# Optimization experiments

Measured on AMD Instinct MI355X. Metric: run time of the kernel, lower is better.

The kernel has to match this reference:

```python
import jax, jax.numpy as jnp
import numpy as np

TEMPERATURE = 0.8
TOP_K = 50
TOP_P = 0.9
REP_PENALTY = 1.2
FILTER_VALUE = -1e9  # stands in for -inf in HF top_k_top_p_filtering (numerically identical probs)

B, S, V = 16, 64, 50257
P = 64  # previously generated tokens per sequence


def setup_inputs() -> dict:
    key = jax.random.key(0)
    k1, k2 = jax.random.split(key)
    logits = jax.random.normal(k1, (B, S, V), dtype=jnp.float32) * 3.0
    prev_tokens = jax.random.randint(k2, (S, P), 0, V)
    return {"logits": logits, "prev_tokens": prev_tokens}


def _repetition_penalty(logits, prev_tokens):
    # logits: [B,S,V], prev_tokens: [S,P]
    gathered = jnp.take_along_axis(logits, prev_tokens[None, :, :], axis=-1)  # [B,S,P]
    all_neg = jnp.all(gathered < 0, axis=0, keepdims=True)                    # [1,S,P]
    penalized = jnp.where(all_neg, gathered * REP_PENALTY, gathered / REP_PENALTY)
    s_idx = jnp.broadcast_to(jnp.arange(S)[:, None], prev_tokens.shape)       # [S,P]
    # scatter back (duplicate indices write identical values -> matches set() semantics)
    return logits.at[:, s_idx, prev_tokens].set(penalized)


def _top_k_top_p_filter(logits):
    # top-k: mask everything below the k-th largest logit
    if TOP_K > 0:
        kth = jax.lax.top_k(logits, TOP_K)[0][..., -1:]                       # [B,S,1]
        logits = jnp.where(logits < kth, FILTER_VALUE, logits)
    # top-p (nucleus): sort descending, mask tokens past cumulative prob TOP_P
    if TOP_P < 1.0:
        sort_idx = jnp.argsort(-logits, axis=-1)                              # [B,S,V]
        sorted_logits = jnp.take_along_axis(logits, sort_idx, axis=-1)
        cum_probs = jnp.cumsum(jax.nn.softmax(sorted_logits, axis=-1), axis=-1)
        remove_sorted = cum_probs > TOP_P
        # shift right so the first token exceeding the threshold is kept
        remove_sorted = jnp.concatenate(
            [jnp.zeros_like(remove_sorted[..., :1]), remove_sorted[..., :-1]], axis=-1)
        inv_idx = jnp.argsort(sort_idx, axis=-1)
        remove = jnp.take_along_axis(remove_sorted, inv_idx, axis=-1)
        logits = jnp.where(remove, FILTER_VALUE, logits)
    return logits


def reference(logits, prev_tokens):
    if REP_PENALTY != 1.0:
        logits = _repetition_penalty(logits, prev_tokens)
    logits = logits / TEMPERATURE
    logits = _top_k_top_p_filter(logits)
    # Categorical(logits=...) normalizes logits; return normalized log-probs
    return jax.nn.log_softmax(logits, axis=-1)
```

## Files before the change

### kernel.cpp

```cpp
#include <hip/hip_runtime.h>
#include <cstdint>
#include <cfloat>
#include <math.h>

#define BB 16
#define SS 64
#define VV 50257
#define PP 64

#define NT 512
#define BINS 2048
#define CAP 1536
#define BMW 1572
#define KCAP 128
#define BCAP 512
#define TRAW 6.0f

typedef float f32x4 __attribute__((ext_vector_type(4)));

__device__ __forceinline__ uint32_t fkey(float f) {
    uint32_t u = __float_as_uint(f);
    return u ^ ((uint32_t)((int32_t)u >> 31) | 0x80000000u);
}
__device__ __forceinline__ float key2f(uint32_t u) {
    uint32_t b = (u & 0x80000000u) ? (u ^ 0x80000000u) : ~u;
    return __uint_as_float(b);
}

__global__ __launch_bounds__(NT)
void sch_kernel(const float* __restrict__ logits,
                const int* __restrict__ prev,
                float* __restrict__ out)
{
    const int r   = blockIdx.x;
    const int b   = r / SS;
    const int s   = r % SS;
    const int tid = threadIdx.x;
    const float* row  = logits + (size_t)r * VV;
    float*       orow = out    + (size_t)r * VV;

    __shared__ uint32_t s_bm[BMW];
    __shared__ float    s_cv[CAP];
    __shared__ int      s_ci[CAP];
    __shared__ uint32_t s_hist[BINS];
    __shared__ uint32_t s_scan[16];
    __shared__ int      s_ptok[PP];
    __shared__ float    s_ppen[PP];
    __shared__ float    s_praw[PP];
    __shared__ int      s_pneg[PP];
    __shared__ float    s_binv[BCAP];
    __shared__ double   s_v64[KCAP];
    __shared__ double   s_e64[KCAP];
    __shared__ int      s_ki[KCAP];
    __shared__ float    s_kof[KCAP];
    __shared__ int    s_cnt, s_cntinv, s_b50, s_need, s_cntb, s_k50, s_kp, s_Kk;
    __shared__ float  s_kth, s_rc;
    __shared__ double s_lse;

    for (int i = tid; i < BMW; i += NT) s_bm[i] = 0u;
    if (tid < PP) s_pneg[tid] = 1;
    if (tid == 0) { s_cnt = 0; s_cntinv = 0; }
    __syncthreads();
    for (int pair = tid; pair < PP * BB; pair += NT) {
        int ti = pair & (PP - 1);
        int b2 = pair >> 6;
        int tok = prev[s * PP + ti];
        float g = logits[((size_t)b2 * SS + s) * (size_t)VV + tok];
        if (g >= 0.f) atomicAnd(&s_pneg[ti], 0);
        if (b2 == b) { s_praw[ti] = g; s_ptok[ti] = tok; }
    }
    __syncthreads();
    if (tid < PP) {
        float gown = s_praw[tid];
        float pen = s_pneg[tid] ? (gown * 1.2f) : (gown / 1.2f);
        s_ppen[tid] = pen;
        int tok = s_ptok[tid];
        atomicOr(&s_bm[tok >> 5], 1u << (tok & 31));
    }
    __syncthreads();

    const int mis   = (int)(((size_t)row >> 2) & 3);
    const int head  = (4 - mis) & 3;
    const int nq    = (VV - head) >> 2;
    const int ttail = head + (nq << 2);
    const float4* p4 = reinterpret_cast<const float4*>(row + head);

    auto kbit = [&](int t) -> uint32_t {
        return (s_bm[t >> 5] >> (t & 31)) & 1u;
    };
    auto addRaw = [&](int t, float raw) {
        if (raw >= TRAW) {
            int pos = atomicAdd(&s_cnt, 1);
            if (pos < CAP) { s_cv[pos] = raw; s_ci[pos] = t; }
        }
    };
    auto streamFast = [&]() {
        for (int t = tid; t < head; t += NT) addRaw(t, row[t]);
        int base = 0;
        for (; base + 4 * NT <= nq; base += 4 * NT) {
            float4 f[4];
            #pragma unroll
            for (int u = 0; u < 4; ++u) f[u] = p4[base + tid + u * NT];
            #pragma unroll
            for (int u = 0; u < 4; ++u) {
                int t = head + ((base + tid + u * NT) << 2);
                addRaw(t + 0, f[u].x);
                addRaw(t + 1, f[u].y);
                addRaw(t + 2, f[u].z);
                addRaw(t + 3, f[u].w);
            }
        }
        for (int q = base + tid; q < nq; q += NT) {
            float4 f = p4[q];
            int t = head + (q << 2);
            addRaw(t + 0, f.x);
            addRaw(t + 1, f.y);
            addRaw(t + 2, f.z);
            addRaw(t + 3, f.w);
        }
        for (int t = ttail + tid; t < VV; t += NT) addRaw(t, row[t]);
    };
    auto procFull = [&](int t, float raw, bool doHist, float thr) {
        float v = raw;
        if (kbit(t)) {
            #pragma unroll 1
            for (int j = 0; j < PP; ++j)
                if (s_ptok[j] == t) { v = s_ppen[j]; break; }
        }
        if (!doHist) {
            if (v >= thr) {
                int pos = atomicAdd(&s_cnt, 1);
                if (pos < CAP) { s_cv[pos] = v; s_ci[pos] = t; }
            }
        } else {
            atomicAdd(&s_hist[fkey(v) >> 21], 1u);
        }
    };
    auto streamFull = [&](bool doHist, float thr) {
        for (int t = tid; t < head; t += NT) procFull(t, row[t], doHist, thr);
        for (int q = tid; q < nq; q += NT) {
            float4 f = p4[q];
            int t = head + (q << 2);
            procFull(t + 0, f.x, doHist, thr);
            procFull(t + 1, f.y, doHist, thr);
            procFull(t + 2, f.z, doHist, thr);
            procFull(t + 3, f.w, doHist, thr);
        }
        for (int t = ttail + tid; t < VV; t += NT) procFull(t, row[t], doHist, thr);
    };
    auto findB50 = [&](int target) {
        __syncthreads();
        const int per = BINS / NT;
        int base = tid * per;
        uint32_t loc = 0;
        #pragma unroll
        for (int k2 = 0; k2 < per; ++k2) loc += s_hist[base + k2];
        uint32_t incl = loc;
        #pragma unroll
        for (int off = 1; off < 64; off <<= 1) {
            uint32_t u = (uint32_t)__shfl_up((int)incl, off, 64);
            if ((tid & 63) >= off) incl += u;
        }
        int wid = tid >> 6;
        if ((tid & 63) == 63) s_scan[wid] = incl;
        __syncthreads();
        if (tid < 8) {
            uint32_t p = 0;
            for (int w = 0; w < tid; ++w) p += s_scan[w];
            s_scan[8 + tid] = p;
        }
        __syncthreads();
        uint32_t pre_incl = s_scan[8 + wid] + incl;
        uint32_t total    = s_scan[8 + 7] + s_scan[7];
        uint32_t run = total - pre_incl;
        for (int k2 = per - 1; k2 >= 0; --k2) {
            uint32_t h = s_hist[base + k2];
            uint32_t run2 = run + h;
            if (run < (uint32_t)target && run2 >= (uint32_t)target) {
                s_b50 = base + k2;
                s_need = target - (int)run;
            }
            run = run2;
        }
        __syncthreads();
    };
    auto doFallback = [&]() {
        for (int i = tid; i < BINS; i += NT) s_hist[i] = 0u;
        __syncthreads();
        streamFull(true, 0.f);
        findB50(50);
        float thrF = key2f((uint32_t)s_b50 << 21);
        if (tid == 0) s_cnt = 0;
        __syncthreads();
        streamFull(false, thrF);
        __syncthreads();
    };
    auto computeKth = [&]() {
        for (int i = tid; i < BINS; i += NT) s_hist[i] = 0u;
        if (tid == 0) { s_cntb = 0; s_kth = -FLT_MAX; }
        __syncthreads();
        int cc = min(s_cnt, CAP);
        for (int i = tid; i < cc; i += NT)
            atomicAdd(&s_hist[fkey(s_cv[i]) >> 21], 1u);
        findB50(50);
        int b50 = s_b50, need = s_need;
        for (int i = tid; i < cc; i += NT) {
            if ((int)(fkey(s_cv[i]) >> 21) == b50) {
                int p = atomicAdd(&s_cntb, 1);
                if (p < BCAP) s_binv[p] = s_cv[i];
            }
        }
        __syncthreads();
        int cb = min(s_cntb, BCAP);
        for (int i = tid; i < cb; i += NT) {
            float vi = s_binv[i];
            int gt = 0, ge = 0;
            for (int j = 0; j < cb; ++j) {
                float vj = s_binv[j];
                gt += (vj > vi);
                ge += (vj >= vi);
            }
            if (gt < need && ge >= need) s_kth = vi;
        }
        __syncthreads();
    };

    streamFast();
    __syncthreads();
    const int cntRaw = min(s_cnt, CAP);
    for (int i = tid; i < cntRaw; i += NT) {
        if (kbit(s_ci[i])) {
            s_cv[i] = -FLT_MAX;
            atomicAdd(&s_cntinv, 1);
        }
    }
    __syncthreads();
    if (tid < PP) {
        int tok = s_ptok[tid];
        bool first = true;
        for (int j = 0; j < tid; ++j)
            if (s_ptok[j] == tok) { first = false; break; }
        if (first) {
            int pos = atomicAdd(&s_cnt, 1);
            if (pos < CAP) { s_cv[pos] = s_ppen[tid]; s_ci[pos] = tok; }
        }
    }
    __syncthreads();
    bool fellback = false;
    {
        bool okc = (s_cnt <= CAP) && ((cntRaw - s_cntinv) >= 50);
        if (!okc) { doFallback(); fellback = true; }
    }

    computeKth();
    if (!fellback && (s_kth - 1e-4f < TRAW)) {
        doFallback();
        computeKth();
    }
    if (tid == 0) s_k50 = 0;
    __syncthreads();
    const float kth = s_kth;

    const float gthr = kth - 1e-4f;
    const int cntc = min(s_cnt, CAP);
    for (int i = tid; i < cntc; i += NT) {
        if (s_cv[i] >= gthr) {
            int p = atomicAdd(&s_k50, 1);
            if (p < KCAP) {
                int tok = s_ci[i];
                double v64;
                if (kbit(tok)) {
                    int pj = 0;
                    #pragma unroll 1
                    for (int j = 0; j < PP; ++j)
                        if (s_ptok[j] == tok) { pj = j; break; }
                    double g = (double)s_praw[pj];
                    double pen = s_pneg[pj] ? (g * 1.2) : (g / 1.2);
                    v64 = pen / 0.8;
                } else {
                    v64 = (double)s_cv[i] / 0.8;
                }
                s_v64[p] = v64;
                s_ki[p]  = tok;
            }
        }
    }
    __syncthreads();
    const int k50c = min(s_k50, KCAP);
    for (int i = k50c + tid; i < KCAP; i += NT) {
        s_v64[i] = -1e300;
        s_ki[i]  = (1 << 30) + i;
    }
    __syncthreads();

    if (tid < 64) {
        int l = tid;
        double v0 = s_v64[l],    v1 = s_v64[l + 64];
        int    i0 = s_ki[l],     i1 = s_ki[l + 64];
        for (int k = 2; k <= KCAP; k <<= 1) {
            for (int j = k >> 1; j > 0; j >>= 1) {
                if (j >= 64) {
                    bool before = (v0 > v1) || (v0 == v1 && i0 < i1);
                    if (!before) {
                        double tv = v0; v0 = v1; v1 = tv;
                        int    ti = i0; i0 = i1; i1 = ti;
                    }
                } else {
                    double nv0 = __shfl_xor(v0, j, 64);
                    double nv1 = __shfl_xor(v1, j, 64);
                    int    ni0 = __shfl_xor(i0, j, 64);
                    int    ni1 = __shfl_xor(i1, j, 64);
                    bool lower = ((l & j) == 0);
                    bool up0 = ((l & k) == 0);
                    bool up1 = (((l + 64) & k) == 0);
                    bool bm0 = (v0 > nv0) || (v0 == nv0 && i0 < ni0);
                    bool bm1 = (v1 > nv1) || (v1 == nv1 && i1 < ni1);
                    bool keep0 = lower ? (up0 == bm0) : (up0 != bm0);
                    bool keep1 = lower ? (up1 == bm1) : (up1 != bm1);
                    if (!keep0) { v0 = nv0; i0 = ni0; }
                    if (!keep1) { v1 = nv1; i1 = ni1; }
                }
            }
        }
        s_v64[l] = v0; s_v64[l + 64] = v1;
        s_ki[l]  = i0; s_ki[l + 64]  = i1;
    }
    __syncthreads();

    if (tid == 0) {
        int kk = k50c;
        int Kkept;
        if (kk <= 50) Kkept = kk;
        else {
            double kth64 = s_v64[49];
            Kkept = 50;
            while (Kkept < kk && s_v64[Kkept] == kth64) ++Kkept;
        }
        s_Kk = Kkept;
    }
    __syncthreads();
    const int Kk = s_Kk;
    const double mx = s_v64[0];
    if (tid < Kk) s_e64[tid] = exp(s_v64[tid] - mx);
    __syncthreads();
    if (tid == 0) {
        double D = 0.0;
        #pragma unroll 1
        for (int i = 0; i < Kk; ++i) D += s_e64[i];
        double c = 0.0;
        int Kp = 0;
        #pragma unroll 1
        for (int i = 0; i < Kk; ++i) {
            bool keep = (i == 0) || (c <= 0.9);
            c += s_e64[i] / D;
            if (keep) Kp = i + 1; else break;
        }
        double D2 = 0.0;
        #pragma unroll 1
        for (int i = 0; i < Kp; ++i) D2 += s_e64[i];
        double lse = log(D2);
        s_lse = lse;
        s_rc = (float)((-1e9 - mx) - lse);
        s_kp = Kp;
    }
    __syncthreads();
    if (tid < s_kp) s_kof[tid] = (float)((s_v64[tid] - mx) - s_lse);

    const float rc = s_rc;
    {
        const int omis   = (int)(((size_t)orow >> 2) & 3);
        const int ohead  = (4 - omis) & 3;
        const int onq    = (VV - ohead) >> 2;
        const int ottail = ohead + (onq << 2);
        f32x4* o4 = reinterpret_cast<f32x4*>(orow + ohead);
        f32x4 rc4; rc4.x = rc; rc4.y = rc; rc4.z = rc; rc4.w = rc;
        for (int t = tid; t < ohead; t += NT)
            __builtin_nontemporal_store(rc, &orow[t]);
        for (int q = tid; q < onq; q += NT)
            __builtin_nontemporal_store(rc4, &o4[q]);
        for (int t = ottail + tid; t < VV; t += NT)
            __builtin_nontemporal_store(rc, &orow[t]);
    }
    __syncthreads();
    if (tid < s_kp) orow[s_ki[tid]] = s_kof[tid];
}

extern "C" void kernel_launch(void* const* d_in, const int* in_sizes, int n_in,
                              void* d_out, int out_size, void* d_ws, size_t ws_size,
                              hipStream_t stream) {
    const float* logits = (const float*)d_in[0];
    const int*   prev   = (const int*)d_in[1];
    float*       out    = (float*)d_out;
    dim3 grid(BB * SS), block(NT);
    hipLaunchKernelGGL(sch_kernel, grid, block, 0, stream, logits, prev, out);
}
```

Measured before the change: 99.40 us.

## Process two rows per block, overlapping row A output stores with row B loads

Each block now handles two rows, rA and rA+512, which share the same sequence index, and the grid shrinks from 1024 to 512 blocks. The repetition-penalty gather for those rows is done once and yields penalties for both. The fill store of row A's output is interleaved with the streaming read and candidate collection of row B, so reads and writes overlap inside one block. In exchange, each block does its work serially across two rows with fewer blocks in flight, which may cut latency hiding and parallelism across the CUs.

```diff
diff --git a/kernel.cpp b/kernel.cpp
--- a/kernel.cpp
+++ b/kernel.cpp
@@ -9,6 +9,7 @@
 #define PP 64
 
 #define NT 512
+#define NBLK 512
 #define BINS 2048
 #define CAP 1536
 #define BMW 1572
@@ -32,12 +33,17 @@
                 const int* __restrict__ prev,
                 float* __restrict__ out)
 {
-    const int r   = blockIdx.x;
-    const int b   = r / SS;
-    const int s   = r % SS;
+    const int g   = blockIdx.x;
+    const int rA  = g;
+    const int rB  = g + NBLK;
+    const int s   = g % SS;
+    const int bA  = rA / SS;
+    const int bB  = rB / SS;
     const int tid = threadIdx.x;
-    const float* row  = logits + (size_t)r * VV;
-    float*       orow = out    + (size_t)r * VV;
+    const float* rowA  = logits + (size_t)rA * VV;
+    const float* rowB  = logits + (size_t)rB * VV;
+    float*       orowA = out    + (size_t)rA * VV;
+    float*       orowB = out    + (size_t)rB * VV;
 
     __shared__ uint32_t s_bm[BMW];
     __shared__ float    s_cv[CAP];
@@ -45,9 +51,11 @@
     __shared__ uint32_t s_hist[BINS];
     __shared__ uint32_t s_scan[16];
     __shared__ int      s_ptok[PP];
-    __shared__ float    s_ppen[PP];
-    __shared__ float    s_praw[PP];
     __shared__ int      s_pneg[PP];
+    __shared__ float    s_prawA[PP];
+    __shared__ float    s_prawB[PP];
+    __shared__ float    s_ppenA[PP];
+    __shared__ float    s_ppenB[PP];
     __shared__ float    s_binv[BCAP];
     __shared__ double   s_v64[KCAP];
     __shared__ double   s_e64[KCAP];
@@ -65,25 +73,22 @@
         int ti = pair & (PP - 1);
         int b2 = pair >> 6;
         int tok = prev[s * PP + ti];
-        float g = logits[((size_t)b2 * SS + s) * (size_t)VV + tok];
-        if (g >= 0.f) atomicAnd(&s_pneg[ti], 0);
-        if (b2 == b) { s_praw[ti] = g; s_ptok[ti] = tok; }
+        float gg = logits[((size_t)b2 * SS + s) * (size_t)VV + tok];
+        if (gg >= 0.f) atomicAnd(&s_pneg[ti], 0);
+        if (b2 == 0)  s_ptok[ti]  = tok;
+        if (b2 == bA) s_prawA[ti] = gg;
+        if (b2 == bB) s_prawB[ti] = gg;
     }
     __syncthreads();
     if (tid < PP) {
-        float gown = s_praw[tid];
-        float pen = s_pneg[tid] ? (gown * 1.2f) : (gown / 1.2f);
-        s_ppen[tid] = pen;
+        int neg = s_pneg[tid];
+        float ga = s_prawA[tid], gb = s_prawB[tid];
+        s_ppenA[tid] = neg ? (ga * 1.2f) : (ga / 1.2f);
+        s_ppenB[tid] = neg ? (gb * 1.2f) : (gb / 1.2f);
         int tok = s_ptok[tid];
         atomicOr(&s_bm[tok >> 5], 1u << (tok & 31));
     }
     __syncthreads();
-
-    const int mis   = (int)(((size_t)row >> 2) & 3);
-    const int head  = (4 - mis) & 3;
-    const int nq    = (VV - head) >> 2;
-    const int ttail = head + (nq << 2);
-    const float4* p4 = reinterpret_cast<const float4*>(row + head);
 
     auto kbit = [&](int t) -> uint32_t {
         return (s_bm[t >> 5] >> (t & 31)) & 1u;
@@ -94,8 +99,13 @@
             if (pos < CAP) { s_cv[pos] = raw; s_ci[pos] = t; }
         }
     };
-    auto streamFast = [&]() {
-        for (int t = tid; t < head; t += NT) addRaw(t, row[t]);
+    auto streamFast = [&](const float* row_) {
+        const int mis   = (int)(((size_t)row_ >> 2) & 3);
+        const int head  = (4 - mis) & 3;
+        const int nq    = (VV - head) >> 2;
+        const int ttail = head + (nq << 2);
+        const float4* p4 = reinterpret_cast<const float4*>(row_ + head);
+        for (int t = tid; t < head; t += NT) addRaw(t, row_[t]);
         int base = 0;
         for (; base + 4 * NT <= nq; base += 4 * NT) {
             float4 f[4];
@@ -113,19 +123,17 @@
         for (int q = base + tid; q < nq; q += NT) {
             float4 f = p4[q];
             int t = head + (q << 2);
-            addRaw(t + 0, f.x);
-            addRaw(t + 1, f.y);
-            addRaw(t + 2, f.z);
-            addRaw(t + 3, f.w);
-        }
-        for (int t = ttail + tid; t < VV; t += NT) addRaw(t, row[t]);
-    };
-    auto procFull = [&](int t, float raw, bool doHist, float thr) {
+            addRaw(t + 0, f.x); addRaw(t + 1, f.y);
+            addRaw(t + 2, f.z); addRaw(t + 3, f.w);
+        }
+        for (int t = ttail + tid; t < VV; t += NT) addRaw(t, row_[t]);
+    };
+    auto procFull = [&](int t, float raw, bool doHist, float thr, const float* ppenS) {
         float v = raw;
         if (kbit(t)) {
             #pragma unroll 1
             for (int j = 0; j < PP; ++j)
-                if (s_ptok[j] == t) { v = s_ppen[j]; break; }
+                if (s_ptok[j] == t) { v = ppenS[j]; break; }
         }
         if (!doHist) {
             if (v >= thr) {
@@ -136,17 +144,22 @@
             atomicAdd(&s_hist[fkey(v) >> 21], 1u);
         }
     };
-    auto streamFull = [&](bool doHist, float thr) {
-        for (int t = tid; t < head; t += NT) procFull(t, row[t], doHist, thr);
+    auto streamFull = [&](bool doHist, float thr, const float* row_, const float* ppenS) {
+        const int mis   = (int)(((size_t)row_ >> 2) & 3);
+        const int head  = (4 - mis) & 3;
+        const int nq    = (VV - head) >> 2;
+        const int ttail = head + (nq << 2);
+        const float4* p4 = reinterpret_cast<const float4*>(row_ + head);
+        for (int t = tid; t < head; t += NT) procFull(t, row_[t], doHist, thr, ppenS);
         for (int q = tid; q < nq; q += NT) {
             float4 f = p4[q];
             int t = head + (q << 2);
-            procFull(t + 0, f.x, doHist, thr);
-            procFull(t + 1, f.y, doHist, thr);
-            procFull(t + 2, f.z, doHist, thr);
-            procFull(t + 3, f.w, doHist, thr);
-        }
-        for (int t = ttail + tid; t < VV; t += NT) procFull(t, row[t], doHist, thr);
+            procFull(t + 0, f.x, doHist, thr, ppenS);
+            procFull(t + 1, f.y, doHist, thr, ppenS);
+            procFull(t + 2, f.z, doHist, thr, ppenS);
+            procFull(t + 3, f.w, doHist, thr, ppenS);
+        }
+        for (int t = ttail + tid; t < VV; t += NT) procFull(t, row_[t], doHist, thr, ppenS);
     };
     auto findB50 = [&](int target) {
         __syncthreads();
@@ -184,15 +197,15 @@
         }
         __syncthreads();
     };
-    auto doFallback = [&]() {
+    auto doFallback = [&](const float* row_, const float* ppenS) {
         for (int i = tid; i < BINS; i += NT) s_hist[i] = 0u;
         __syncthreads();
-        streamFull(true, 0.f);
+        streamFull(true, 0.f, row_, ppenS);
         findB50(50);
         float thrF = key2f((uint32_t)s_b50 << 21);
         if (tid == 0) s_cnt = 0;
         __syncthreads();
-        streamFull(false, thrF);
+        streamFull(false, thrF, row_, ppenS);
         __syncthreads();
     };
     auto computeKth = [&]() {
@@ -225,164 +238,223 @@
         __syncthreads();
     };
 
-    streamFast();
-    __syncthreads();
-    const int cntRaw = min(s_cnt, CAP);
-    for (int i = tid; i < cntRaw; i += NT) {
-        if (kbit(s_ci[i])) {
-            s_cv[i] = -FLT_MAX;
-            atomicAdd(&s_cntinv, 1);
-        }
-    }
-    __syncthreads();
-    if (tid < PP) {
-        int tok = s_ptok[tid];
-        bool first = true;
-        for (int j = 0; j < tid; ++j)
-            if (s_ptok[j] == tok) { first = false; break; }
-        if (first) {
-            int pos = atomicAdd(&s_cnt, 1);
-            if (pos < CAP) { s_cv[pos] = s_ppen[tid]; s_ci[pos] = tok; }
-        }
-    }
-    __syncthreads();
-    bool fellback = false;
+    auto midPhases = [&](const float* row_, const float* prawS, const float* ppenS) {
+        const int cntRaw = min(s_cnt, CAP);
+        for (int i = tid; i < cntRaw; i += NT) {
+            if (kbit(s_ci[i])) {
+                s_cv[i] = -FLT_MAX;
+                atomicAdd(&s_cntinv, 1);
+            }
+        }
+        __syncthreads();
+        if (tid < PP) {
+            int tok = s_ptok[tid];
+            bool first = true;
+            for (int j = 0; j < tid; ++j)
+                if (s_ptok[j] == tok) { first = false; break; }
+            if (first) {
+                int pos = atomicAdd(&s_cnt, 1);
+                if (pos < CAP) { s_cv[pos] = ppenS[tid]; s_ci[pos] = tok; }
+            }
+        }
+        __syncthreads();
+        bool fellback = false;
+        {
+            bool okc = (s_cnt <= CAP) && ((cntRaw - s_cntinv) >= 50);
+            if (!okc) { doFallback(row_, ppenS); fellback = true; }
+        }
+        computeKth();
+        if (!fellback && (s_kth - 1e-4f < TRAW)) {
+            doFallback(row_, ppenS);
+            computeKth();
+        }
+        if (tid == 0) s_k50 = 0;
+        __syncthreads();
+        const float gthr = s_kth - 1e-4f;
+        const int cntc = min(s_cnt, CAP);
+        for (int i = tid; i < cntc; i += NT) {
+            if (s_cv[i] >= gthr) {
+                int p = atomicAdd(&s_k50, 1);
+                if (p < KCAP) {
+                    int tok = s_ci[i];
+                    double v64;
+                    if (kbit(tok)) {
+                        int pj = 0;
+                        #pragma unroll 1
+                        for (int j = 0; j < PP; ++j)
+                            if (s_ptok[j] == tok) { pj = j; break; }
+                        double gd = (double)prawS[pj];
+                        double pen = s_pneg[pj] ? (gd * 1.2) : (gd / 1.2);
+                        v64 = pen / 0.8;
+                    } else {
+                        v64 = (double)s_cv[i] / 0.8;
+                    }
+                    s_v64[p] = v64;
+                    s_ki[p]  = tok;
+                }
+            }
+        }
+        __syncthreads();
+        const int k50c = min(s_k50, KCAP);
+        for (int i = k50c + tid; i < KCAP; i += NT) {
+            s_v64[i] = -1e300;
+            s_ki[i]  = (1 << 30) + i;
+        }
+        __syncthreads();
+        if (tid < 64) {
+            int l = tid;
+            double v0 = s_v64[l],    v1 = s_v64[l + 64];
+            int    i0 = s_ki[l],     i1 = s_ki[l + 64];
+            for (int k = 2; k <= KCAP; k <<= 1) {
+                for (int j = k >> 1; j > 0; j >>= 1) {
+                    if (j >= 64) {
+                        bool before = (v0 > v1) || (v0 == v1 && i0 < i1);
+                        if (!before) {
+                            double tv = v0; v0 = v1; v1 = tv;
+                            int    ti = i0; i0 = i1; i1 = ti;
+                        }
+                    } else {
+                        double nv0 = __shfl_xor(v0, j, 64);
+                        double nv1 = __shfl_xor(v1, j, 64);
+                        int    ni0 = __shfl_xor(i0, j, 64);
+                        int    ni1 = __shfl_xor(i1, j, 64);
+                        bool lower = ((l & j) == 0);
+                        bool up0 = ((l & k) == 0);
+                        bool up1 = (((l + 64) & k) == 0);
+                        bool bm0 = (v0 > nv0) || (v0 == nv0 && i0 < ni0);
+                        bool bm1 = (v1 > nv1) || (v1 == nv1 && i1 < ni1);
+                        bool keep0 = lower ? (up0 == bm0) : (up0 != bm0);
+                        bool keep1 = lower ? (up1 == bm1) : (up1 != bm1);
+                        if (!keep0) { v0 = nv0; i0 = ni0; }
+                        if (!keep1) { v1 = nv1; i1 = ni1; }
+                    }
+                }
+            }
+            s_v64[l] = v0; s_v64[l + 64] = v1;
+            s_ki[l]  = i0; s_ki[l + 64]  = i1;
+        }
+        __syncthreads();
+        if (tid == 0) {
+            int kk = k50c;
+            int Kkept;
+            if (kk <= 50) Kkept = kk;
+            else {
+                double kth64 = s_v64[49];
+                Kkept = 50;
+                while (Kkept < kk && s_v64[Kkept] == kth64) ++Kkept;
+            }
+            s_Kk = Kkept;
+        }
+        __syncthreads();
+        const int Kk = s_Kk;
+        const double mx = s_v64[0];
+        if (tid < Kk) s_e64[tid] = exp(s_v64[tid] - mx);
+        __syncthreads();
+        if (tid == 0) {
+            double D = 0.0;
+            #pragma unroll 1
+            for (int i = 0; i < Kk; ++i) D += s_e64[i];
+            double c = 0.0;
+            int Kp = 0;
+            #pragma unroll 1
+            for (int i = 0; i < Kk; ++i) {
+                bool keep = (i == 0) || (c <= 0.9);
+                c += s_e64[i] / D;
+                if (keep) Kp = i + 1; else break;
+            }
+            double D2 = 0.0;
+            #pragma unroll 1
+            for (int i = 0; i < Kp; ++i) D2 += s_e64[i];
+            double lse = log(D2);
+            s_lse = lse;
+            s_rc = (float)((-1e9 - mx) - lse);
+            s_kp = Kp;
+        }
+        __syncthreads();
+        if (tid < s_kp) s_kof[tid] = (float)((s_v64[tid] - mx) - s_lse);
+        __syncthreads();
+    };
+
+    streamFast(rowA);
+    __syncthreads();
+    midPhases(rowA, s_prawA, s_ppenA);
+    const int   kpA = s_kp;
+    const float rcA = s_rc;
+    if (tid == 0) { s_cnt = 0; s_cntinv = 0; }
+    __syncthreads();
+
     {
-        bool okc = (s_cnt <= CAP) && ((cntRaw - s_cntinv) >= 50);
-        if (!okc) { doFallback(); fellback = true; }
-    }
-
-    computeKth();
-    if (!fellback && (s_kth - 1e-4f < TRAW)) {
-        doFallback();
-        computeKth();
-    }
-    if (tid == 0) s_k50 = 0;
-    __syncthreads();
-    const float kth = s_kth;
-
-    const float gthr = kth - 1e-4f;
-    const int cntc = min(s_cnt, CAP);
-    for (int i = tid; i < cntc; i += NT) {
-        if (s_cv[i] >= gthr) {
-            int p = atomicAdd(&s_k50, 1);
-            if (p < KCAP) {
-                int tok = s_ci[i];
-                double v64;
-                if (kbit(tok)) {
-                    int pj = 0;
-                    #pragma unroll 1
-                    for (int j = 0; j < PP; ++j)
-                        if (s_ptok[j] == tok) { pj = j; break; }
-                    double g = (double)s_praw[pj];
-                    double pen = s_pneg[pj] ? (g * 1.2) : (g / 1.2);
-                    v64 = pen / 0.8;
-                } else {
-                    v64 = (double)s_cv[i] / 0.8;
-                }
-                s_v64[p] = v64;
-                s_ki[p]  = tok;
-            }
-        }
-    }
-    __syncthreads();
-    const int k50c = min(s_k50, KCAP);
-    for (int i = k50c + tid; i < KCAP; i += NT) {
-        s_v64[i] = -1e300;
-        s_ki[i]  = (1 << 30) + i;
-    }
-    __syncthreads();
-
-    if (tid < 64) {
-        int l = tid;
-        double v0 = s_v64[l],    v1 = s_v64[l + 64];
-        int    i0 = s_ki[l],     i1 = s_ki[l + 64];
-        for (int k = 2; k <= KCAP; k <<= 1) {
-            for (int j = k >> 1; j > 0; j >>= 1) {
-                if (j >= 64) {
-                    bool before = (v0 > v1) || (v0 == v1 && i0 < i1);
-                    if (!before) {
-                        double tv = v0; v0 = v1; v1 = tv;
-                        int    ti = i0; i0 = i1; i1 = ti;
-                    }
-                } else {
-                    double nv0 = __shfl_xor(v0, j, 64);
-                    double nv1 = __shfl_xor(v1, j, 64);
-                    int    ni0 = __shfl_xor(i0, j, 64);
-                    int    ni1 = __shfl_xor(i1, j, 64);
-                    bool lower = ((l & j) == 0);
-                    bool up0 = ((l & k) == 0);
-                    bool up1 = (((l + 64) & k) == 0);
-                    bool bm0 = (v0 > nv0) || (v0 == nv0 && i0 < ni0);
-                    bool bm1 = (v1 > nv1) || (v1 == nv1 && i1 < ni1);
-                    bool keep0 = lower ? (up0 == bm0) : (up0 != bm0);
-                    bool keep1 = lower ? (up1 == bm1) : (up1 != bm1);
-                    if (!keep0) { v0 = nv0; i0 = ni0; }
-                    if (!keep1) { v1 = nv1; i1 = ni1; }
-                }
-            }
-        }
-        s_v64[l] = v0; s_v64[l + 64] = v1;
-        s_ki[l]  = i0; s_ki[l + 64]  = i1;
-    }
-    __syncthreads();
-
-    if (tid == 0) {
-        int kk = k50c;
-        int Kkept;
-        if (kk <= 50) Kkept = kk;
-        else {
-            double kth64 = s_v64[49];
-            Kkept = 50;
-            while (Kkept < kk && s_v64[Kkept] == kth64) ++Kkept;
-        }
-        s_Kk = Kkept;
-    }
-    __syncthreads();
-    const int Kk = s_Kk;
-    const double mx = s_v64[0];
-    if (tid < Kk) s_e64[tid] = exp(s_v64[tid] - mx);
-    __syncthreads();
-    if (tid == 0) {
-        double D = 0.0;
-        #pragma unroll 1
-        for (int i = 0; i < Kk; ++i) D += s_e64[i];
-        double c = 0.0;
-        int Kp = 0;
-        #pragma unroll 1
-        for (int i = 0; i < Kk; ++i) {
-            bool keep = (i == 0) || (c <= 0.9);
-            c += s_e64[i] / D;
-            if (keep) Kp = i + 1; else break;
-        }
-        double D2 = 0.0;
-        #pragma unroll 1
-        for (int i = 0; i < Kp; ++i) D2 += s_e64[i];
-        double lse = log(D2);
-        s_lse = lse;
-        s_rc = (float)((-1e9 - mx) - lse);
-        s_kp = Kp;
-    }
-    __syncthreads();
-    if (tid < s_kp) s_kof[tid] = (float)((s_v64[tid] - mx) - s_lse);
-
-    const float rc = s_rc;
-    {
-        const int omis   = (int)(((size_t)orow >> 2) & 3);
+        const int omis   = (int)(((size_t)orowA >> 2) & 3);
         const int ohead  = (4 - omis) & 3;
         const int onq    = (VV - ohead) >> 2;
         const int ottail = ohead + (onq << 2);
-        f32x4* o4 = reinterpret_cast<f32x4*>(orow + ohead);
-        f32x4 rc4; rc4.x = rc; rc4.y = rc; rc4.z = rc; rc4.w = rc;
+        f32x4* o4 = reinterpret_cast<f32x4*>(orowA + ohead);
+        f32x4 rc4; rc4.x = rcA; rc4.y = rcA; rc4.z = rcA; rc4.w = rcA;
+
+        const int mis   = (int)(((size_t)rowB >> 2) & 3);
+        const int head  = (4 - mis) & 3;
+        const int nq    = (VV - head) >> 2;
+        const int ttail = head + (nq << 2);
+        const float4* p4 = reinterpret_cast<const float4*>(rowB + head);
+
         for (int t = tid; t < ohead; t += NT)
-            __builtin_nontemporal_store(rc, &orow[t]);
+            __builtin_nontemporal_store(rcA, &orowA[t]);
+        for (int t = tid; t < head; t += NT) addRaw(t, rowB[t]);
+
+        const int common = min(onq, nq);
+        int base = 0;
+        for (; base + 2 * NT <= common; base += 2 * NT) {
+            float4 f0 = p4[base + tid];
+            float4 f1 = p4[base + tid + NT];
+            __builtin_nontemporal_store(rc4, &o4[base + tid]);
+            __builtin_nontemporal_store(rc4, &o4[base + tid + NT]);
+            int t0 = head + ((base + tid) << 2);
+            int t1 = head + ((base + tid + NT) << 2);
+            addRaw(t0 + 0, f0.x); addRaw(t0 + 1, f0.y);
+            addRaw(t0 + 2, f0.z); addRaw(t0 + 3, f0.w);
+            addRaw(t1 + 0, f1.x); addRaw(t1 + 1, f1.y);
+            addRaw(t1 + 2, f1.z); addRaw(t1 + 3, f1.w);
+        }
+        for (int q = base + tid; q < common; q += NT) {
+            float4 f = p4[q];
+            __builtin_nontemporal_store(rc4, &o4[q]);
+            int t = head + (q << 2);
+            addRaw(t + 0, f.x); addRaw(t + 1, f.y);
+            addRaw(t + 2, f.z); addRaw(t + 3, f.w);
+        }
+        for (int q = common + tid; q < onq; q += NT)
+            __builtin_nontemporal_store(rc4, &o4[q]);
+        for (int q = common + tid; q < nq; q += NT) {
+            float4 f = p4[q];
+            int t = head + (q << 2);
+            addRaw(t + 0, f.x); addRaw(t + 1, f.y);
+            addRaw(t + 2, f.z); addRaw(t + 3, f.w);
+        }
+        for (int t = ottail + tid; t < VV; t += NT)
+            __builtin_nontemporal_store(rcA, &orowA[t]);
+        for (int t = ttail + tid; t < VV; t += NT) addRaw(t, rowB[t]);
+    }
+    __syncthreads();
+    if (tid < kpA) orowA[s_ki[tid]] = s_kof[tid];
+
+    midPhases(rowB, s_prawB, s_ppenB);
+    {
+        const float rcB = s_rc;
+        const int omis   = (int)(((size_t)orowB >> 2) & 3);
+        const int ohead  = (4 - omis) & 3;
+        const int onq    = (VV - ohead) >> 2;
+        const int ottail = ohead + (onq << 2);
+        f32x4* o4 = reinterpret_cast<f32x4*>(orowB + ohead);
+        f32x4 rc4; rc4.x = rcB; rc4.y = rcB; rc4.z = rcB; rc4.w = rcB;
+        for (int t = tid; t < ohead; t += NT)
+            __builtin_nontemporal_store(rcB, &orowB[t]);
         for (int q = tid; q < onq; q += NT)
             __builtin_nontemporal_store(rc4, &o4[q]);
         for (int t = ottail + tid; t < VV; t += NT)
-            __builtin_nontemporal_store(rc, &orow[t]);
+            __builtin_nontemporal_store(rcB, &orowB[t]);
     }
     __syncthreads();
-    if (tid < s_kp) orow[s_ki[tid]] = s_kof[tid];
+    if (tid < s_kp) orowB[s_ki[tid]] = s_kof[tid];
 }
 
 extern "C" void kernel_launch(void* const* d_in, const int* in_sizes, int n_in,
@@ -391,6 +463,6 @@
     const float* logits = (const float*)d_in[0];
     const int*   prev   = (const int*)d_in[1];
     float*       out    = (float*)d_out;
-    dim3 grid(BB * SS), block(NT);
+    dim3 grid(NBLK), block(NT);
     hipLaunchKernelGGL(sch_kernel, grid, block, 0, stream, logits, prev, out);
 }
```

After: 107.7 us. +8.3%, slower.
